# Kernel tuning notes

Hardware: AMD Instinct MI355X
Metric: run time of the kernel (lower is better)

Reference implementation:

```python
import jax, jax.numpy as jnp
import numpy as np

N_WINDOWS = 4
WIN_H, WIN_W = 512, 512          # module 'size'
IMG_H, IMG_W = 1024, 1024        # 2x2 tiling of windows
N_MASKS = 32                     # n_windows * masks_per_window
MPW = N_MASKS // N_WINDOWS       # 8 masks per window (channel 0 of each block = background)
SLOT_DIM = 64
SIM_THRESH = 0.1                 # module 'similarity'


def setup_inputs() -> dict:
    key = jax.random.key(0)
    k1, k2 = jax.random.split(key)
    masks = jax.random.normal(k1, (1, N_MASKS, IMG_H, IMG_W), dtype=jnp.float32)
    slot_features = jax.random.normal(k2, (N_WINDOWS, MPW - 1, SLOT_DIM), dtype=jnp.float32)
    # static window layout, equivalent to keys ['w_0_0','w_512_0','w_0_512','w_512_512']
    pad_left = jnp.array([0, WIN_W, 0, WIN_W], dtype=jnp.int32)
    pad_top = jnp.array([0, 0, WIN_H, WIN_H], dtype=jnp.int32)
    return {"masks": masks, "slot_features": slot_features,
            "pad_left": pad_left, "pad_top": pad_top}


def _merge_windows(masks, slot_features, pl, pt):
    """pl, pt: python int lists (static metadata parsed from keys)."""
    B, C, H, W = masks.shape
    mpw = C // N_WINDOWS

    # --- to_one_hot: argmax over channel dim, one-hot back to [B,C,H,W] float ---
    ids = jnp.argmax(masks, axis=1)                                   # [B,H,W]
    m = jnp.moveaxis(jax.nn.one_hot(ids, C, dtype=masks.dtype), -1, 1)  # [B,C,H,W]

    ranges = [(i * mpw, (i + 1) * mpw) for i in range(N_WINDOWS)]

    # --- adjacency over window pads (static) ---
    adjacency = []
    for i in range(N_WINDOWS):
        for j in range(i + 1, N_WINDOWS):
            if pt[i] == pt[j] and abs(pl[i] - pl[j]) == WIN_W:
                adjacency.append((i, j, True) if pl[i] < pl[j] else (j, i, True))
            if pl[i] == pl[j] and abs(pt[i] - pt[j]) == WIN_H:
                adjacency.append((i, j, False) if pt[i] < pt[j] else (j, i, False))

    # --- per-channel edge-touch booleans (vectorized replacement of set building) ---
    edge_l = jnp.zeros((C,), bool)
    edge_r = jnp.zeros((C,), bool)
    edge_t = jnp.zeros((C,), bool)
    edge_b = jnp.zeros((C,), bool)
    for wi, (s, e) in enumerate(ranges):
        ys, ye = max(pt[wi], 0), min(pt[wi] + WIN_H, H)
        xs, xe = max(pl[wi], 0), min(pl[wi] + WIN_W, W)
        if ys >= ye or xs >= xe:
            continue
        win = m[0, s:e, ys:ye, xs:xe]                # [mpw, hh, ww]
        edge_l = edge_l.at[s:e].set(jnp.any(win[:, :, 0] == 1, axis=-1))
        edge_r = edge_r.at[s:e].set(jnp.any(win[:, :, -1] == 1, axis=-1))
        edge_t = edge_t.at[s:e].set(jnp.any(win[:, 0, :] == 1, axis=-1))
        edge_b = edge_b.at[s:e].set(jnp.any(win[:, -1, :] == 1, axis=-1))

    # --- static candidate pair list (background channels ci % mpw == 0 excluded) ---
    ci_l, cj_l, wi_l, wj_l, hz_l = [], [], [], [], []
    for wi, wj, horiz in adjacency:
        si, ei = ranges[wi]
        sj, ej = ranges[wj]
        for ci in range(si + 1, ei):
            for cj in range(sj + 1, ej):
                ci_l.append(ci); cj_l.append(cj)
                wi_l.append(wi); wj_l.append(wj); hz_l.append(horiz)
    P = len(ci_l)
    if P == 0:
        return m

    ci_a = jnp.array(ci_l, jnp.int32)
    cj_a = jnp.array(cj_l, jnp.int32)
    horiz = jnp.array(hz_l)

    # --- cosine similarities for all pairs at once ---
    sf_n = slot_features / (jnp.linalg.norm(slot_features, axis=-1, keepdims=True) + 1e-8)
    rel_i = np.array(ci_l) % mpw - 1
    rel_j = np.array(cj_l) % mpw - 1
    fi = sf_n[np.array(wi_l), rel_i]                 # [P, D]
    fj = sf_n[np.array(wj_l), rel_j]
    sims = jnp.sum(fi * fj, axis=-1)                 # [P]

    edge_ok = jnp.where(horiz, edge_r[ci_a] & edge_l[cj_a], edge_b[ci_a] & edge_t[cj_a])
    passing = edge_ok & (sims > SIM_THRESH)          # [P]

    # --- sequential dedup/merge scan (order-dependent, like the torch loop) ---
    def step(carry, xs):
        m, merged = carry
        ci, cj, ok = xs
        cond = ok & ~merged[ci] & ~merged[cj]
        keep = jnp.minimum(ci, cj)
        rem = jnp.maximum(ci, cj)
        rem_ch = jnp.take(m, rem, axis=1)            # [B,H,W]
        m = m.at[:, keep].add(jnp.where(cond, rem_ch, 0.0))
        m = m.at[:, rem].set(jnp.where(cond, jnp.zeros_like(rem_ch), rem_ch))
        merged = merged.at[rem].set(merged[rem] | cond)
        return (m, merged), None

    (m, _), _ = jax.lax.scan(step, (m, jnp.zeros((C,), bool)), (ci_a, cj_a, passing))
    return m


def reference(masks, slot_features, pad_left, pad_top):
    # pads encode the (static) window layout parsed from the string keys
    pl = [int(v) for v in np.asarray(pad_left)]
    pt = [int(v) for v in np.asarray(pad_top)]
    return _merge_windows(masks, slot_features, pl, pt)
```

## Files before the change

kernel.cpp:

```cpp
#include <hip/hip_runtime.h>

#define IMG_H 1024
#define IMG_W 1024
#define NPIX (IMG_H * IMG_W)
#define N_MASKS 32
#define N_WINDOWS 4
#define MPW 8
#define WIN_H 512
#define WIN_W 512
#define SIM_THRESH 0.1f

#define WS_EDGE 0
#define WS_LOC  64
#define WS_IDS  256

__global__ void k_init(unsigned* e) {
    if (threadIdx.x < 4) e[threadIdx.x] = 0u;
}

template <bool STORE_IDS>
__global__ __launch_bounds__(256) void k_argmax(const float* __restrict__ masks,
                                                const int* __restrict__ pl,
                                                const int* __restrict__ pt,
                                                unsigned* __restrict__ edge_masks,
                                                unsigned char* __restrict__ ids) {
    __shared__ int spl[4], spt[4];
    if (threadIdx.x < 4) { spl[threadIdx.x] = pl[threadIdx.x]; spt[threadIdx.x] = pt[threadIdx.x]; }
    __syncthreads();

    int t = blockIdx.x * blockDim.x + threadIdx.x;
    int idx = t * 4;
    if (idx >= NPIX) return;

    float bv[4];
    int bc[4];
    {
        const float4 v = *(const float4*)(masks + idx);
        bv[0] = v.x; bv[1] = v.y; bv[2] = v.z; bv[3] = v.w;
        bc[0] = bc[1] = bc[2] = bc[3] = 0;
    }
#pragma unroll
    for (int c = 1; c < N_MASKS; c++) {
        const float4 v = *(const float4*)(masks + (size_t)c * NPIX + idx);
        if (v.x > bv[0]) { bv[0] = v.x; bc[0] = c; }
        if (v.y > bv[1]) { bv[1] = v.y; bc[1] = c; }
        if (v.z > bv[2]) { bv[2] = v.z; bc[2] = c; }
        if (v.w > bv[3]) { bv[3] = v.w; bc[3] = c; }
    }

    if (STORE_IDS) {
        uchar4 o;
        o.x = (unsigned char)bc[0]; o.y = (unsigned char)bc[1];
        o.z = (unsigned char)bc[2]; o.w = (unsigned char)bc[3];
        *(uchar4*)(ids + idx) = o;
    }

    int y = idx >> 10;
    int x0 = idx & (IMG_W - 1);
#pragma unroll
    for (int wi = 0; wi < N_WINDOWS; wi++) {
        int xs = max(spl[wi], 0), xe = min(spl[wi] + WIN_W, IMG_W);
        int ys = max(spt[wi], 0), ye = min(spt[wi] + WIN_H, IMG_H);
        if (ys >= ye || xs >= xe) continue;
        if (y < ys || y >= ye) continue;
#pragma unroll
        for (int k = 0; k < 4; k++) {
            int x = x0 + k;
            if (x < xs || x >= xe) continue;
            int c = bc[k];
            if ((c >> 3) != wi) continue;
            unsigned bit = 1u << c;
            if (x == xs)     atomicOr(&edge_masks[0], bit);
            if (x == xe - 1) atomicOr(&edge_masks[1], bit);
            if (y == ys)     atomicOr(&edge_masks[2], bit);
            if (y == ye - 1) atomicOr(&edge_masks[3], bit);
        }
    }
}

__global__ __launch_bounds__(64) void k_merge(const float* __restrict__ sf,
                                              const int* __restrict__ pl,
                                              const int* __restrict__ pt,
                                              const unsigned* __restrict__ edge_masks,
                                              int* __restrict__ loc_out) {
    __shared__ float sfn[N_WINDOWS * (MPW - 1) * 64];
    __shared__ unsigned char pci[640], pcj[640], phz[640], pass_[640];
    __shared__ int sP;
    int lane = threadIdx.x;

    for (int r = 0; r < N_WINDOWS * (MPW - 1); r++) {
        float v = sf[r * 64 + lane];
        float s = v * v;
#pragma unroll
        for (int off = 1; off < 64; off <<= 1) s += __shfl_xor(s, off, 64);
        sfn[r * 64 + lane] = v * (1.0f / (sqrtf(s) + 1e-8f));
    }
    __syncthreads();

    if (lane == 0) {
        int lpl[4], lpt[4];
        for (int i = 0; i < 4; i++) { lpl[i] = pl[i]; lpt[i] = pt[i]; }
        int aI[12], aJ[12], aH[12], na = 0;
        for (int i = 0; i < N_WINDOWS; i++)
            for (int j = i + 1; j < N_WINDOWS; j++) {
                if (lpt[i] == lpt[j] && abs(lpl[i] - lpl[j]) == WIN_W) {
                    if (lpl[i] < lpl[j]) { aI[na] = i; aJ[na] = j; }
                    else                 { aI[na] = j; aJ[na] = i; }
                    aH[na] = 1; na++;
                }
                if (lpl[i] == lpl[j] && abs(lpt[i] - lpt[j]) == WIN_H) {
                    if (lpt[i] < lpt[j]) { aI[na] = i; aJ[na] = j; }
                    else                 { aI[na] = j; aJ[na] = i; }
                    aH[na] = 0; na++;
                }
            }
        int P = 0;
        for (int a = 0; a < na; a++)
            for (int ci = aI[a] * MPW + 1; ci < (aI[a] + 1) * MPW; ci++)
                for (int cj = aJ[a] * MPW + 1; cj < (aJ[a] + 1) * MPW; cj++) {
                    pci[P] = (unsigned char)ci;
                    pcj[P] = (unsigned char)cj;
                    phz[P] = (unsigned char)aH[a];
                    P++;
                }
        sP = P;
    }
    __syncthreads();

    int P = sP;
    unsigned el = edge_masks[0], er = edge_masks[1], et = edge_masks[2], eb = edge_masks[3];
    for (int p = lane; p < P; p += 64) {
        int ci = pci[p], cj = pcj[p];
        int wi = ci >> 3, wj = cj >> 3;
        const float* fi = &sfn[(wi * (MPW - 1) + (ci & 7) - 1) * 64];
        const float* fj = &sfn[(wj * (MPW - 1) + (cj & 7) - 1) * 64];
        float s = 0.f;
#pragma unroll
        for (int k = 0; k < 64; k++) s += fi[k] * fj[k];
        bool eok = phz[p] ? (((er >> ci) & 1u) && ((el >> cj) & 1u))
                          : (((eb >> ci) & 1u) && ((et >> cj) & 1u));
        pass_[p] = (eok && s > SIM_THRESH) ? 1 : 0;
    }
    __syncthreads();

    if (lane == 0) {
        int loc[32];
        unsigned merged = 0;
        for (int c = 0; c < 32; c++) loc[c] = c;
        for (int p = 0; p < P; p++) {
            int ci = pci[p], cj = pcj[p];
            if (pass_[p] && !((merged >> ci) & 1u) && !((merged >> cj) & 1u)) {
                int keep = min(ci, cj), rem = max(ci, cj);
                for (int o = 0; o < 32; o++)
                    if (loc[o] == rem) loc[o] = keep;
                merged |= 1u << rem;
            }
        }
        for (int c = 0; c < 32; c++) loc_out[c] = loc[c];
    }
}

__global__ __launch_bounds__(256) void k_write(const unsigned char* __restrict__ ids,
                                               const int* __restrict__ loc_g,
                                               float* __restrict__ out) {
    __shared__ int loc[32];
    if (threadIdx.x < 32) loc[threadIdx.x] = loc_g[threadIdx.x];
    __syncthreads();

    int t = blockIdx.x * blockDim.x + threadIdx.x;
    int idx = t * 4;
    if (idx >= NPIX) return;

    uchar4 id4 = *(const uchar4*)(ids + idx);
    int r0 = loc[id4.x], r1 = loc[id4.y], r2 = loc[id4.z], r3 = loc[id4.w];
#pragma unroll
    for (int c = 0; c < N_MASKS; c++) {
        float4 v;
        v.x = (r0 == c) ? 1.0f : 0.0f;
        v.y = (r1 == c) ? 1.0f : 0.0f;
        v.z = (r2 == c) ? 1.0f : 0.0f;
        v.w = (r3 == c) ? 1.0f : 0.0f;
        *(float4*)(out + (size_t)c * NPIX + idx) = v;
    }
}

__global__ __launch_bounds__(256) void k_write_recompute(const float* __restrict__ masks,
                                                         const int* __restrict__ loc_g,
                                                         float* __restrict__ out) {
    __shared__ int loc[32];
    if (threadIdx.x < 32) loc[threadIdx.x] = loc_g[threadIdx.x];
    __syncthreads();

    int t = blockIdx.x * blockDim.x + threadIdx.x;
    int idx = t * 4;
    if (idx >= NPIX) return;

    float bv[4];
    int bc[4];
    {
        const float4 v = *(const float4*)(masks + idx);
        bv[0] = v.x; bv[1] = v.y; bv[2] = v.z; bv[3] = v.w;
        bc[0] = bc[1] = bc[2] = bc[3] = 0;
    }
#pragma unroll
    for (int c = 1; c < N_MASKS; c++) {
        const float4 v = *(const float4*)(masks + (size_t)c * NPIX + idx);
        if (v.x > bv[0]) { bv[0] = v.x; bc[0] = c; }
        if (v.y > bv[1]) { bv[1] = v.y; bc[1] = c; }
        if (v.z > bv[2]) { bv[2] = v.z; bc[2] = c; }
        if (v.w > bv[3]) { bv[3] = v.w; bc[3] = c; }
    }
    int r0 = loc[bc[0]], r1 = loc[bc[1]], r2 = loc[bc[2]], r3 = loc[bc[3]];
#pragma unroll
    for (int c = 0; c < N_MASKS; c++) {
        float4 v;
        v.x = (r0 == c) ? 1.0f : 0.0f;
        v.y = (r1 == c) ? 1.0f : 0.0f;
        v.z = (r2 == c) ? 1.0f : 0.0f;
        v.w = (r3 == c) ? 1.0f : 0.0f;
        *(float4*)(out + (size_t)c * NPIX + idx) = v;
    }
}

extern "C" void kernel_launch(void* const* d_in, const int* in_sizes, int n_in,
                              void* d_out, int out_size, void* d_ws, size_t ws_size,
                              hipStream_t stream) {
    const float* masks = (const float*)d_in[0];
    const float* sf    = (const float*)d_in[1];
    const int*   pl    = (const int*)d_in[2];
    const int*   pt    = (const int*)d_in[3];
    float* out = (float*)d_out;

    char* ws = (char*)d_ws;
    unsigned* edge_masks = (unsigned*)(ws + WS_EDGE);
    int* loc = (int*)(ws + WS_LOC);
    unsigned char* ids = (unsigned char*)(ws + WS_IDS);

    const bool have_ids_ws = (ws_size >= (size_t)(WS_IDS + NPIX));

    const int nthreads = NPIX / 4;
    const int blocks = nthreads / 256;

    k_init<<<1, 64, 0, stream>>>(edge_masks);

    if (have_ids_ws) {
        k_argmax<true><<<blocks, 256, 0, stream>>>(masks, pl, pt, edge_masks, ids);
        k_merge<<<1, 64, 0, stream>>>(sf, pl, pt, edge_masks, loc);
        k_write<<<blocks, 256, 0, stream>>>(ids, loc, out);
    } else {
        k_argmax<false><<<blocks, 256, 0, stream>>>(masks, pl, pt, edge_masks, nullptr);
        k_merge<<<1, 64, 0, stream>>>(sf, pl, pt, edge_masks, loc);
        k_write_recompute<<<blocks, 256, 0, stream>>>(masks, loc, out);
    }
}
```

Baseline: 281.9 us.

## Replace global edge atomics with per-block partials, drop init kernel, nontemporal stores

Edge-touch bits are now accumulated in shared memory per block and written as per-block words, which the merge kernel OR-reduces, so the separate init kernel and global atomics are no longer needed. The merge kernel packs step metadata into single words, pads the feature array to avoid bank conflicts, and runs the sequential merge scan in parallel, with each lane tracking one channel. The output write uses nontemporal stores to reduce cache pollution on the 128MB output. The fallback path that recomputed argmax when the workspace was too small is removed, so the code now assumes a workspace of about 1MB.

New measurement: 275.5 us. -2.3%, faster.

```diff
diff --git a/kernel.cpp b/kernel.cpp
--- a/kernel.cpp
+++ b/kernel.cpp
@@ -9,98 +9,105 @@
 #define WIN_H 512
 #define WIN_W 512
 #define SIM_THRESH 0.1f
-
-#define WS_EDGE 0
-#define WS_LOC  64
-#define WS_IDS  256
-
-__global__ void k_init(unsigned* e) {
-    if (threadIdx.x < 4) e[threadIdx.x] = 0u;
-}
-
-template <bool STORE_IDS>
+#define NBLK 1024
+
+typedef float vf4 __attribute__((ext_vector_type(4)));
+
+#define WS_LOC   0
+#define WS_EDGE  128
+#define WS_IDS   (WS_EDGE + NBLK * 16)
+
 __global__ __launch_bounds__(256) void k_argmax(const float* __restrict__ masks,
                                                 const int* __restrict__ pl,
                                                 const int* __restrict__ pt,
-                                                unsigned* __restrict__ edge_masks,
+                                                uint4* __restrict__ edge_blocks,
                                                 unsigned char* __restrict__ ids) {
     __shared__ int spl[4], spt[4];
-    if (threadIdx.x < 4) { spl[threadIdx.x] = pl[threadIdx.x]; spt[threadIdx.x] = pt[threadIdx.x]; }
-    __syncthreads();
-
-    int t = blockIdx.x * blockDim.x + threadIdx.x;
-    int idx = t * 4;
-    if (idx >= NPIX) return;
-
-    float bv[4];
-    int bc[4];
+    __shared__ unsigned sem[4];
+    const int tid = threadIdx.x;
+    if (tid < 4) { spl[tid] = pl[tid]; spt[tid] = pt[tid]; sem[tid] = 0u; }
+    __syncthreads();
+
+    const int idx = (blockIdx.x * 256 + tid) * 4;
+
+    float bv0, bv1, bv2, bv3;
+    int bc0 = 0, bc1 = 0, bc2 = 0, bc3 = 0;
     {
         const float4 v = *(const float4*)(masks + idx);
-        bv[0] = v.x; bv[1] = v.y; bv[2] = v.z; bv[3] = v.w;
-        bc[0] = bc[1] = bc[2] = bc[3] = 0;
+        bv0 = v.x; bv1 = v.y; bv2 = v.z; bv3 = v.w;
     }
 #pragma unroll
     for (int c = 1; c < N_MASKS; c++) {
         const float4 v = *(const float4*)(masks + (size_t)c * NPIX + idx);
-        if (v.x > bv[0]) { bv[0] = v.x; bc[0] = c; }
-        if (v.y > bv[1]) { bv[1] = v.y; bc[1] = c; }
-        if (v.z > bv[2]) { bv[2] = v.z; bc[2] = c; }
-        if (v.w > bv[3]) { bv[3] = v.w; bc[3] = c; }
-    }
-
-    if (STORE_IDS) {
-        uchar4 o;
-        o.x = (unsigned char)bc[0]; o.y = (unsigned char)bc[1];
-        o.z = (unsigned char)bc[2]; o.w = (unsigned char)bc[3];
-        *(uchar4*)(ids + idx) = o;
-    }
-
-    int y = idx >> 10;
-    int x0 = idx & (IMG_W - 1);
+        if (v.x > bv0) { bv0 = v.x; bc0 = c; }
+        if (v.y > bv1) { bv1 = v.y; bc1 = c; }
+        if (v.z > bv2) { bv2 = v.z; bc2 = c; }
+        if (v.w > bv3) { bv3 = v.w; bc3 = c; }
+    }
+    *(uchar4*)(ids + idx) = make_uchar4((unsigned char)bc0, (unsigned char)bc1,
+                                        (unsigned char)bc2, (unsigned char)bc3);
+
+    const int y = idx >> 10;
+    const int x0 = idx & (IMG_W - 1);
+    const int bcs[4] = {bc0, bc1, bc2, bc3};
 #pragma unroll
     for (int wi = 0; wi < N_WINDOWS; wi++) {
-        int xs = max(spl[wi], 0), xe = min(spl[wi] + WIN_W, IMG_W);
-        int ys = max(spt[wi], 0), ye = min(spt[wi] + WIN_H, IMG_H);
+        const int xs = max(spl[wi], 0), xe = min(spl[wi] + WIN_W, IMG_W);
+        const int ys = max(spt[wi], 0), ye = min(spt[wi] + WIN_H, IMG_H);
         if (ys >= ye || xs >= xe) continue;
         if (y < ys || y >= ye) continue;
 #pragma unroll
         for (int k = 0; k < 4; k++) {
-            int x = x0 + k;
+            const int x = x0 + k;
             if (x < xs || x >= xe) continue;
-            int c = bc[k];
+            const int c = bcs[k];
             if ((c >> 3) != wi) continue;
-            unsigned bit = 1u << c;
-            if (x == xs)     atomicOr(&edge_masks[0], bit);
-            if (x == xe - 1) atomicOr(&edge_masks[1], bit);
-            if (y == ys)     atomicOr(&edge_masks[2], bit);
-            if (y == ye - 1) atomicOr(&edge_masks[3], bit);
+            const unsigned bit = 1u << c;
+            if (x == xs)     atomicOr(&sem[0], bit);
+            if (x == xe - 1) atomicOr(&sem[1], bit);
+            if (y == ys)     atomicOr(&sem[2], bit);
+            if (y == ye - 1) atomicOr(&sem[3], bit);
         }
     }
+    __syncthreads();
+    if (tid == 0) edge_blocks[blockIdx.x] = make_uint4(sem[0], sem[1], sem[2], sem[3]);
 }
 
 __global__ __launch_bounds__(64) void k_merge(const float* __restrict__ sf,
                                               const int* __restrict__ pl,
                                               const int* __restrict__ pt,
-                                              const unsigned* __restrict__ edge_masks,
+                                              const uint4* __restrict__ edge_blocks,
                                               int* __restrict__ loc_out) {
-    __shared__ float sfn[N_WINDOWS * (MPW - 1) * 64];
-    __shared__ unsigned char pci[640], pcj[640], phz[640], pass_[640];
+    __shared__ float sfn[28 * 65];
+    __shared__ unsigned step_word[512];
     __shared__ int sP;
-    int lane = threadIdx.x;
+    const int lane = threadIdx.x;
+
+    unsigned el = 0, er = 0, et = 0, eb = 0;
+    for (int b = lane; b < NBLK; b += 64) {
+        const uint4 w = edge_blocks[b];
+        el |= w.x; er |= w.y; et |= w.z; eb |= w.w;
+    }
+#pragma unroll
+    for (int off = 1; off < 64; off <<= 1) {
+        el |= __shfl_xor(el, off);
+        er |= __shfl_xor(er, off);
+        et |= __shfl_xor(et, off);
+        eb |= __shfl_xor(eb, off);
+    }
 
     for (int r = 0; r < N_WINDOWS * (MPW - 1); r++) {
-        float v = sf[r * 64 + lane];
+        const float v = sf[r * 64 + lane];
         float s = v * v;
 #pragma unroll
-        for (int off = 1; off < 64; off <<= 1) s += __shfl_xor(s, off, 64);
-        sfn[r * 64 + lane] = v * (1.0f / (sqrtf(s) + 1e-8f));
-    }
-    __syncthreads();
+        for (int off = 1; off < 64; off <<= 1) s += __shfl_xor(s, off);
+        sfn[r * 65 + lane] = v * (1.0f / (sqrtf(s) + 1e-8f));
+    }
 
     if (lane == 0) {
         int lpl[4], lpt[4];
         for (int i = 0; i < 4; i++) { lpl[i] = pl[i]; lpt[i] = pt[i]; }
-        int aI[12], aJ[12], aH[12], na = 0;
+        int aI[8], aJ[8], aH[8], na = 0;
         for (int i = 0; i < N_WINDOWS; i++)
             for (int j = i + 1; j < N_WINDOWS; j++) {
                 if (lpt[i] == lpt[j] && abs(lpl[i] - lpl[j]) == WIN_W) {
@@ -117,47 +124,42 @@
         int P = 0;
         for (int a = 0; a < na; a++)
             for (int ci = aI[a] * MPW + 1; ci < (aI[a] + 1) * MPW; ci++)
-                for (int cj = aJ[a] * MPW + 1; cj < (aJ[a] + 1) * MPW; cj++) {
-                    pci[P] = (unsigned char)ci;
-                    pcj[P] = (unsigned char)cj;
-                    phz[P] = (unsigned char)aH[a];
-                    P++;
-                }
+                for (int cj = aJ[a] * MPW + 1; cj < (aJ[a] + 1) * MPW; cj++)
+                    step_word[P++] = (unsigned)ci | ((unsigned)cj << 8)
+                                   | ((unsigned)aH[a] << 16);
         sP = P;
     }
     __syncthreads();
 
-    int P = sP;
-    unsigned el = edge_masks[0], er = edge_masks[1], et = edge_masks[2], eb = edge_masks[3];
+    const int P = sP;
     for (int p = lane; p < P; p += 64) {
-        int ci = pci[p], cj = pcj[p];
-        int wi = ci >> 3, wj = cj >> 3;
-        const float* fi = &sfn[(wi * (MPW - 1) + (ci & 7) - 1) * 64];
-        const float* fj = &sfn[(wj * (MPW - 1) + (cj & 7) - 1) * 64];
+        const unsigned w = step_word[p];
+        const int ci = w & 255, cj = (w >> 8) & 255, hz = (w >> 16) & 1;
+        const float* fi = &sfn[((ci >> 3) * (MPW - 1) + (ci & 7) - 1) * 65];
+        const float* fj = &sfn[((cj >> 3) * (MPW - 1) + (cj & 7) - 1) * 65];
         float s = 0.f;
 #pragma unroll
         for (int k = 0; k < 64; k++) s += fi[k] * fj[k];
-        bool eok = phz[p] ? (((er >> ci) & 1u) && ((el >> cj) & 1u))
-                          : (((eb >> ci) & 1u) && ((et >> cj) & 1u));
-        pass_[p] = (eok && s > SIM_THRESH) ? 1 : 0;
-    }
-    __syncthreads();
-
-    if (lane == 0) {
-        int loc[32];
-        unsigned merged = 0;
-        for (int c = 0; c < 32; c++) loc[c] = c;
-        for (int p = 0; p < P; p++) {
-            int ci = pci[p], cj = pcj[p];
-            if (pass_[p] && !((merged >> ci) & 1u) && !((merged >> cj) & 1u)) {
-                int keep = min(ci, cj), rem = max(ci, cj);
-                for (int o = 0; o < 32; o++)
-                    if (loc[o] == rem) loc[o] = keep;
+        const bool eok = hz ? (((er >> ci) & 1u) && ((el >> cj) & 1u))
+                            : (((eb >> ci) & 1u) && ((et >> cj) & 1u));
+        if (eok && s > SIM_THRESH) step_word[p] = w | (1u << 17);
+    }
+    __syncthreads();
+
+    unsigned merged = 0;
+    int myloc = lane;
+    for (int p = 0; p < P; p++) {
+        const unsigned w = step_word[p];
+        if (w >> 17) {
+            const int ci = w & 255, cj = (w >> 8) & 255;
+            if (!((merged >> ci) & 1u) && !((merged >> cj) & 1u)) {
+                const int keep = min(ci, cj), rem = max(ci, cj);
+                if (myloc == rem) myloc = keep;
                 merged |= 1u << rem;
             }
         }
-        for (int c = 0; c < 32; c++) loc_out[c] = loc[c];
-    }
+    }
+    if (lane < 32) loc_out[lane] = myloc;
 }
 
 __global__ __launch_bounds__(256) void k_write(const unsigned char* __restrict__ ids,
@@ -167,58 +169,17 @@
     if (threadIdx.x < 32) loc[threadIdx.x] = loc_g[threadIdx.x];
     __syncthreads();
 
-    int t = blockIdx.x * blockDim.x + threadIdx.x;
-    int idx = t * 4;
-    if (idx >= NPIX) return;
-
-    uchar4 id4 = *(const uchar4*)(ids + idx);
-    int r0 = loc[id4.x], r1 = loc[id4.y], r2 = loc[id4.z], r3 = loc[id4.w];
+    const int idx = (blockIdx.x * 256 + threadIdx.x) * 4;
+    const uchar4 id4 = *(const uchar4*)(ids + idx);
+    const int r0 = loc[id4.x], r1 = loc[id4.y], r2 = loc[id4.z], r3 = loc[id4.w];
 #pragma unroll
     for (int c = 0; c < N_MASKS; c++) {
-        float4 v;
+        vf4 v;
         v.x = (r0 == c) ? 1.0f : 0.0f;
         v.y = (r1 == c) ? 1.0f : 0.0f;
         v.z = (r2 == c) ? 1.0f : 0.0f;
         v.w = (r3 == c) ? 1.0f : 0.0f;
-        *(float4*)(out + (size_t)c * NPIX + idx) = v;
-    }
-}
-
-__global__ __launch_bounds__(256) void k_write_recompute(const float* __restrict__ masks,
-                                                         const int* __restrict__ loc_g,
-                                                         float* __restrict__ out) {
-    __shared__ int loc[32];
-    if (threadIdx.x < 32) loc[threadIdx.x] = loc_g[threadIdx.x];
-    __syncthreads();
-
-    int t = blockIdx.x * blockDim.x + threadIdx.x;
-    int idx = t * 4;
-    if (idx >= NPIX) return;
-
-    float bv[4];
-    int bc[4];
-    {
-        const float4 v = *(const float4*)(masks + idx);
-        bv[0] = v.x; bv[1] = v.y; bv[2] = v.z; bv[3] = v.w;
-        bc[0] = bc[1] = bc[2] = bc[3] = 0;
-    }
-#pragma unroll
-    for (int c = 1; c < N_MASKS; c++) {
-        const float4 v = *(const float4*)(masks + (size_t)c * NPIX + idx);
-        if (v.x > bv[0]) { bv[0] = v.x; bc[0] = c; }
-        if (v.y > bv[1]) { bv[1] = v.y; bc[1] = c; }
-        if (v.z > bv[2]) { bv[2] = v.z; bc[2] = c; }
-        if (v.w > bv[3]) { bv[3] = v.w; bc[3] = c; }
-    }
-    int r0 = loc[bc[0]], r1 = loc[bc[1]], r2 = loc[bc[2]], r3 = loc[bc[3]];
-#pragma unroll
-    for (int c = 0; c < N_MASKS; c++) {
-        float4 v;
-        v.x = (r0 == c) ? 1.0f : 0.0f;
-        v.y = (r1 == c) ? 1.0f : 0.0f;
-        v.z = (r2 == c) ? 1.0f : 0.0f;
-        v.w = (r3 == c) ? 1.0f : 0.0f;
-        *(float4*)(out + (size_t)c * NPIX + idx) = v;
+        __builtin_nontemporal_store(v, (vf4*)(out + (size_t)c * NPIX + idx));
     }
 }
 
@@ -232,24 +193,11 @@
     float* out = (float*)d_out;
 
     char* ws = (char*)d_ws;
-    unsigned* edge_masks = (unsigned*)(ws + WS_EDGE);
     int* loc = (int*)(ws + WS_LOC);
+    uint4* edge_blocks = (uint4*)(ws + WS_EDGE);
     unsigned char* ids = (unsigned char*)(ws + WS_IDS);
 
-    const bool have_ids_ws = (ws_size >= (size_t)(WS_IDS + NPIX));
-
-    const int nthreads = NPIX / 4;
-    const int blocks = nthreads / 256;
-
-    k_init<<<1, 64, 0, stream>>>(edge_masks);
-
-    if (have_ids_ws) {
-        k_argmax<true><<<blocks, 256, 0, stream>>>(masks, pl, pt, edge_masks, ids);
-        k_merge<<<1, 64, 0, stream>>>(sf, pl, pt, edge_masks, loc);
-        k_write<<<blocks, 256, 0, stream>>>(ids, loc, out);
-    } else {
-        k_argmax<false><<<blocks, 256, 0, stream>>>(masks, pl, pt, edge_masks, nullptr);
-        k_merge<<<1, 64, 0, stream>>>(sf, pl, pt, edge_masks, loc);
-        k_write_recompute<<<blocks, 256, 0, stream>>>(masks, loc, out);
-    }
-}
+    k_argmax<<<NBLK, 256, 0, stream>>>(masks, pl, pt, edge_blocks, ids);
+    k_merge<<<1, 64, 0, stream>>>(sf, pl, pt, edge_blocks, loc);
+    k_write<<<NBLK, 256, 0, stream>>>(ids, loc, out);
+}
```
